# Kernel tuning notes

Measured on AMD Instinct MI355X. Metric: run time of the kernel, lower is better.

Reference implementation:

```python
import jax, jax.numpy as jnp
import numpy as np

H = 1024        # rnn_hidden
E = 128         # label_emb_dim
L = 17          # num_labels
START = L       # start-of-sequence label id


def setup_inputs() -> dict:
    key = jax.random.key(0)
    ks = jax.random.split(key, 8)
    B, T = 256, 512
    seg_encodings = jax.random.normal(ks[0], (B, T, H), jnp.float32)
    labels = jax.random.randint(ks[1], (B, T), 0, L, dtype=jnp.int32)
    def init(k, shape, fan_in):
        return (jax.random.normal(k, shape, jnp.float32) / np.sqrt(fan_in)).astype(jnp.float32)
    emb_table = init(ks[2], (L + 1, E), E)          # label_emb.weight
    W_ih = init(ks[3], (3 * H, H + E), H + E)        # gru.weight_ih_l0 (r,z,n)
    W_hh = init(ks[4], (3 * H, H), H)                # gru.weight_hh_l0
    b_ih = jnp.zeros((3 * H,), jnp.float32)
    b_hh = jnp.zeros((3 * H,), jnp.float32)
    W_out = init(ks[5], (L, H), H)                   # out.weight
    b_out = jnp.zeros((L,), jnp.float32)
    return {"seg_encodings": seg_encodings, "labels": labels,
            "emb_table": emb_table, "W_ih": W_ih, "W_hh": W_hh,
            "b_ih": b_ih, "b_hh": b_hh, "W_out": W_out, "b_out": b_out}


def reference(seg_encodings, labels, emb_table, W_ih, W_hh, b_ih, b_hh, W_out, b_out):
    B, T, _ = seg_encodings.shape
    # teacher forcing: prev label at step t is labels[:, t-1], START at t=0
    prev = jnp.concatenate([jnp.full((B, 1), START, labels.dtype), labels[:, :-1]], axis=1)
    prev_emb = emb_table[prev]                                  # [B,T,E]
    x = jnp.concatenate([seg_encodings, prev_emb], axis=-1)     # [B,T,H+E]
    # hoist the input projection out of the recurrence: one big GEMM
    x_proj = jnp.einsum('bti,gi->btg', x, W_ih) + b_ih          # [B,T,3H]

    def step(h, xp):                                            # h:[B,H], xp:[B,3H]
        gh = h @ W_hh.T + b_hh                                  # [B,3H]
        xr, xz, xn = jnp.split(xp, 3, axis=-1)
        hr, hz, hn = jnp.split(gh, 3, axis=-1)
        r = jax.nn.sigmoid(xr + hr)
        z = jax.nn.sigmoid(xz + hz)
        n = jnp.tanh(xn + r * hn)
        h_new = (1.0 - z) * n + z * h
        return h_new, h_new

    h0 = jnp.zeros((B, H), seg_encodings.dtype)
    _, hs = jax.lax.scan(step, h0, jnp.swapaxes(x_proj, 0, 1))  # hs: [T,B,H]
    hs = jnp.swapaxes(hs, 0, 1)                                 # [B,T,H]
    logits = jnp.einsum('bth,lh->btl', hs, W_out) + b_out       # [B,T,L]
    return logits
```

## Files before the change

### kernel.cpp

```cpp
#include <hip/hip_runtime.h>
#include <hip/hip_fp16.h>

typedef unsigned short u16;
typedef unsigned int u32;
typedef unsigned long long u64;

#define NT 512
#define NB 256
#define NH 1024
#define NE 128
#define NHE 1152
#define NL 17
#define MT 8
#define JTILES 32
#define XKC 36
#define HKC 32
#define KCT 68
#define NBLK 256
#define THREADS 512

typedef __attribute__((ext_vector_type(8))) _Float16 half8;
typedef __attribute__((ext_vector_type(4))) float f32x4;

#define WS_CNT     0ull
#define WS_HBUF    4096ull
#define WS_WPACK   1052672ull
#define WS_WOPACK  14422016ull
#define WS_XPACK   14487552ull
#define WS_TOTAL   316477440ull

#define HB_U64_PER (HKC * 2 * 64 * 2)
#define XSLOT_U16  (XKC * 2 * 64 * 8)

__device__ __forceinline__ u16 f2h(float f) {
  __half h = __float2half(f);
  return __builtin_bit_cast(u16, h);
}
__device__ __forceinline__ float h2f(u16 u) {
  return __half2float(__builtin_bit_cast(__half, u));
}
__device__ __forceinline__ uint4 pack8h(const u16* o) {
  uint4 v;
  v.x = (u32)o[0] | ((u32)o[1] << 16);
  v.y = (u32)o[2] | ((u32)o[3] << 16);
  v.z = (u32)o[4] | ((u32)o[5] << 16);
  v.w = (u32)o[6] | ((u32)o[7] << 16);
  return v;
}

__device__ __forceinline__ void gll16u(const void* g, void* l) {
  __builtin_amdgcn_global_load_lds((const __attribute__((address_space(1))) u32*)g,
                                   (__attribute__((address_space(3))) u32*)l, 16, 0, 17);
}
__device__ __forceinline__ void gll16c(const void* g, void* l) {
  __builtin_amdgcn_global_load_lds((const __attribute__((address_space(1))) u32*)g,
                                   (__attribute__((address_space(3))) u32*)l, 16, 0, 0);
}

__global__ void zero_ws(uint4* p) {
  int idx = blockIdx.x * 256 + threadIdx.x;
  if (idx < 33024) {
    uint4 z; z.x = 0; z.y = 0; z.z = 0; z.w = 0;
    p[idx] = z;
  }
}

__global__ void pack_w(const float* __restrict__ Wih, const float* __restrict__ Whh,
                       const float* __restrict__ Wout, u16* __restrict__ wpack,
                       u16* __restrict__ wopack) {
  int idx = blockIdx.x * 256 + threadIdx.x;
  const int WUNITS = JTILES * KCT * 3 * 2 * 64;
  if (idx < WUNITS) {
    int l = idx & 63;
    int r = idx >> 6;
    int ni = r & 1; r >>= 1;
    int g = r % 3;  r /= 3;
    int kc = r % KCT; r /= KCT;
    int jt = r;
    int row = g * NH + jt * 32 + ni * 16 + (l & 15);
    int kk = (l >> 4) * 8;
    const float* src = (kc < XKC) ? (Wih + (size_t)row * NHE + kc * 32 + kk)
                                  : (Whh + (size_t)row * NH + (kc - XKC) * 32 + kk);
    u16 o[8];
#pragma unroll
    for (int e = 0; e < 8; ++e) o[e] = f2h(src[e]);
    ((uint4*)wpack)[idx] = pack8h(o);
  } else if (idx < WUNITS + HKC * 2 * 64) {
    int j = idx - WUNITS;
    int l = j & 63; j >>= 6;
    int ni = j & 1; int kc = j >> 1;
    int col = (l & 15) + 16 * ni;
    int kk = kc * 32 + (l >> 4) * 8;
    u16 o[8];
#pragma unroll
    for (int e = 0; e < 8; ++e)
      o[e] = (col < NL) ? f2h(Wout[(size_t)col * NH + kk + e]) : (u16)0;
    ((uint4*)wopack)[idx - WUNITS] = pack8h(o);
  }
}

__global__ void pack_x(const float* __restrict__ seg, const int* __restrict__ labels,
                       const float* __restrict__ emb, u16* __restrict__ xpack) {
  __shared__ float ls[32][65];
  __shared__ int lbl[32];
  const int bid = blockIdx.x;
  const int t = bid & (NT - 1);
  const int m = bid >> 9;
  const int tid = threadIdx.x;
  u16* outb = xpack + (size_t)(m * NT + t) * XSLOT_U16;
  const int r = tid >> 3, qq = tid & 7;
  const int l = tid & 63;

  for (int kc2 = 0; kc2 < 16; ++kc2) {
    const float* s = seg + ((size_t)(m * 32 + r) * NT + t) * NH + kc2 * 64 + qq * 8;
    float4 a = ((const float4*)s)[0];
    float4 b2 = ((const float4*)s)[1];
    ls[r][qq * 8 + 0] = a.x;  ls[r][qq * 8 + 1] = a.y;
    ls[r][qq * 8 + 2] = a.z;  ls[r][qq * 8 + 3] = a.w;
    ls[r][qq * 8 + 4] = b2.x; ls[r][qq * 8 + 5] = b2.y;
    ls[r][qq * 8 + 6] = b2.z; ls[r][qq * 8 + 7] = b2.w;
    __syncthreads();
    const int sub2 = tid >> 6;
    const int kc = kc2 * 2 + (sub2 >> 1);
    const int sub = sub2 & 1;
    const int row = sub * 16 + (l & 15);
    const int c0 = (sub2 >> 1) * 32 + (l >> 4) * 8;
    u16 o[8];
#pragma unroll
    for (int e = 0; e < 8; ++e) o[e] = f2h(ls[row][c0 + e]);
    ((uint4*)outb)[(kc * 2 + sub) * 64 + l] = pack8h(o);
    __syncthreads();
  }
  if (tid < 32)
    lbl[tid] = (t == 0) ? NL : labels[(size_t)(m * 32 + tid) * NT + (t - 1)];
  __syncthreads();
#pragma unroll
  for (int k = 0; k < 2; ++k) {
    int u = tid + k * 256;
    int kc = 32 + (u >> 7);
    int sub = (u >> 6) & 1;
    int ll = u & 63;
    int row = sub * 16 + (ll & 15);
    int c = (kc - 32) * 32 + (ll >> 4) * 8;
    const float* s = emb + (size_t)lbl[row] * NE + c;
    float4 a = ((const float4*)s)[0];
    float4 b2 = ((const float4*)s)[1];
    u16 o[8];
    o[0] = f2h(a.x); o[1] = f2h(a.y); o[2] = f2h(a.z); o[3] = f2h(a.w);
    o[4] = f2h(b2.x); o[5] = f2h(b2.y); o[6] = f2h(b2.z); o[7] = f2h(b2.w);
    ((uint4*)outb)[(kc * 2 + sub) * 64 + ll] = pack8h(o);
  }
}

#define MFMA16(a, b, c) __builtin_amdgcn_mfma_f32_16x16x32_f16((a), (b), (c), 0, 0, 0)

#define WAIT_FLAGS(tgt) do { \
  while (true) { \
    u32 v_ = __hip_atomic_load(fl + (l & 31), __ATOMIC_RELAXED, __HIP_MEMORY_SCOPE_AGENT); \
    if (__all((int)v_ >= (tgt))) break; \
  } \
} while (0)

#define ISSUE_X(tt) do { \
  const char* xgb_ = (const char*)xpack + (size_t)(m * NT + (tt)) * (XSLOT_U16 * 2); \
  _Pragma("unroll") \
  for (int k_ = 0; k_ < 9; ++k_) \
    gll16c(xgb_ + ((size_t)(k_ * 512 + tid)) * 16, (void*)(xlds + (k_ * 512 + w * 64))); \
} while (0)

__global__ __launch_bounds__(THREADS, 1)
void gru_persist(u16* xpack, const u16* __restrict__ wpack,
                 const float* __restrict__ bih, const float* __restrict__ bhh,
                 u64* __restrict__ hbuf, u32* __restrict__ counters) {
  __shared__ uint4 hlds[HKC * 2 * 64];
  __shared__ uint4 xlds[XKC * 2 * 64];
  __shared__ u32 glds16[8 * 2 * 2 * 2 * 64];
  __shared__ u16 hbf[32 * 40];

  const int bid = blockIdx.x;
  const int xcd = bid & 7;
  const int q = bid >> 3;
  const int m = q & 7;
  const int jslot = q >> 3;
  const int jt = jslot * 8 + xcd;
  const int tid = threadIdx.x;
  const int w = tid >> 6, l = tid & 63;
  const int l15 = l & 15, l4 = l >> 4;
  const int usub = (w >> 1) & 1, uni = w & 1;

  const uint4* wp = (const uint4*)wpack;
  u32* fl = counters + m * 64;
  const size_t wbase_u = (size_t)jt * (KCT * 6 * 64);

  const int ocol = jt * 32 + uni * 16 + l15;
  const float br = bih[ocol] + bhh[ocol];
  const float bz = bih[NH + ocol] + bhh[NH + ocol];
  const float bxn = bih[2 * NH + ocol];
  const float bhn = bhh[2 * NH + ocol];
  float hold[4] = {0.f, 0.f, 0.f, 0.f};
  const f32x4 z4 = {0.f, 0.f, 0.f, 0.f};

  int tg, tkc0, tkcn; bool tIsX;
  if (w == 6)      { tg = 2; tIsX = true;  tkc0 = 0;  tkcn = 36; }
  else if (w == 7) { tg = 2; tIsX = false; tkc0 = 0;  tkcn = 32; }
  else {
    tg = (w < 3) ? 0 : 1;
    const int r_ = (w < 3) ? w : (w - 3);
    tIsX = (r_ < 2);
    tkc0 = (r_ == 1) ? 18 : 0;
    tkcn = tIsX ? ((r_ == 0) ? 18 : 36) : 32;
  }
  const int tkadd = tIsX ? 0 : XKC;
  const uint4* asrc = tIsX ? xlds : hlds;

  const int a_sub = (tid >> 7) & 1, a_half = (tid >> 6) & 1, a_l = tid & 63;
  const size_t a_off = ((size_t)(jt * 2 + a_sub) * 64 + a_l) * 2 + a_half;

  ISSUE_X(0);

  for (int t = 0; t < NT; ++t) {
    const int par = t & 1;

    WAIT_FLAGS(t);

    {
      const char* gb = (const char*)hbuf + ((size_t)(par * MT + m) * HB_U64_PER) * 8;
#pragma unroll
      for (int k = 0; k < 8; ++k)
        gll16u(gb + ((size_t)(k * 512 + tid)) * 16, (void*)(hlds + (k * 512 + w * 64)));
      asm volatile("s_waitcnt vmcnt(0)" ::: "memory");
      __syncthreads();
    }

    if (t > 0 && tid < 256) {
      const u64 v = ((const u64*)hlds)[a_off];
      u64* dst = (u64*)(xpack + (size_t)(m * NT + (t - 1)) * XSLOT_U16);
      dst[a_off] = v;
    }

    f32x4 acc[2][2];
    acc[0][0] = z4; acc[0][1] = z4; acc[1][0] = z4; acc[1][1] = z4;
#pragma unroll 4
    for (int kc = tkc0; kc < tkcn; ++kc) {
      const int kcw = kc + tkadd;
      uint4 A0 = asrc[(kc * 2 + 0) * 64 + l];
      uint4 A1 = asrc[(kc * 2 + 1) * 64 + l];
      uint4 B0 = wp[wbase_u + (size_t)((kcw * 3 + tg) * 2 + 0) * 64 + l];
      uint4 B1 = wp[wbase_u + (size_t)((kcw * 3 + tg) * 2 + 1) * 64 + l];
      half8 a0 = __builtin_bit_cast(half8, A0);
      half8 a1 = __builtin_bit_cast(half8, A1);
      half8 b0 = __builtin_bit_cast(half8, B0);
      half8 b1 = __builtin_bit_cast(half8, B1);
      acc[0][0] = MFMA16(a0, b0, acc[0][0]);
      acc[0][1] = MFMA16(a0, b1, acc[0][1]);
      acc[1][0] = MFMA16(a1, b0, acc[1][0]);
      acc[1][1] = MFMA16(a1, b1, acc[1][1]);
    }

#pragma unroll
    for (int s = 0; s < 2; ++s)
#pragma unroll
      for (int n = 0; n < 2; ++n)
#pragma unroll
        for (int rgp = 0; rgp < 2; ++rgp) {
          u32 v = (u32)f2h(acc[s][n][rgp * 2]) |
                  ((u32)f2h(acc[s][n][rgp * 2 + 1]) << 16);
          glds16[((((w * 2 + s) * 2 + n) * 2 + rgp)) * 64 + l] = v;
        }
    __syncthreads();

    if (w < 4) {
      float gv[8][4];
#pragma unroll
      for (int task = 0; task < 8; ++task)
#pragma unroll
        for (int rgp = 0; rgp < 2; ++rgp) {
          u32 v = glds16[((((task * 2 + usub) * 2 + uni) * 2 + rgp)) * 64 + l];
          gv[task][rgp * 2]     = h2f((u16)v);
          gv[task][rgp * 2 + 1] = h2f((u16)(v >> 16));
        }
#pragma unroll
      for (int rg = 0; rg < 4; ++rg) {
        float R   = gv[0][rg] + gv[1][rg] + gv[2][rg] + br;
        float Z   = gv[3][rg] + gv[4][rg] + gv[5][rg] + bz;
        float XNv = gv[6][rg] + bxn;
        float HNv = gv[7][rg] + bhn;
        float r_ = 1.f / (1.f + __expf(-R));
        float z_ = 1.f / (1.f + __expf(-Z));
        float pre = XNv + r_ * HNv;
        float e2 = __expf(2.f * pre);
        float n_ = 1.f - 2.f / (e2 + 1.f);
        float hn_ = (1.f - z_) * n_ + z_ * hold[rg];
        hold[rg] = hn_;
        hbf[(usub * 16 + l4 * 4 + rg) * 40 + uni * 16 + l15] = f2h(hn_);
      }
    }
    __syncthreads();

    if (w < 2) {
      const int row = w * 16 + l15;
      const uint4 hv = *(const uint4*)&hbf[(size_t)row * 40 + l4 * 8];
      u64 lo = ((u64)hv.y << 32) | (u64)hv.x;
      u64 hi = ((u64)hv.w << 32) | (u64)hv.z;
      u64* dst = hbuf + (size_t)((par ^ 1) * MT + m) * HB_U64_PER
                      + ((size_t)(jt * 2 + w) * 64 + l) * 2;
      __hip_atomic_store(dst, lo, __ATOMIC_RELAXED, __HIP_MEMORY_SCOPE_AGENT);
      __hip_atomic_store(dst + 1, hi, __ATOMIC_RELAXED, __HIP_MEMORY_SCOPE_AGENT);
    }
    asm volatile("s_waitcnt vmcnt(0)" ::: "memory");
    __syncthreads();
    if (tid == 0)
      __hip_atomic_store(fl + jt, (u32)(t + 1), __ATOMIC_RELAXED, __HIP_MEMORY_SCOPE_AGENT);

    if (t + 1 < NT) ISSUE_X(t + 1);
  }
}

__global__ __launch_bounds__(256, 1)
void logits_pass(const u16* __restrict__ harch, const u64* __restrict__ hbuf,
                 const u16* __restrict__ wopack, const float* __restrict__ bout,
                 float* __restrict__ out) {
  __shared__ uint4 hlds[HKC * 2 * 64];
  __shared__ f32x4 redv[4 * 3 * 64];
  const int bid = blockIdx.x;
  const int m = bid >> 9;
  const int s = bid & 511;
  const int tid = threadIdx.x;
  const int w = tid >> 6, l = tid & 63;
  const int l15 = l & 15, l4 = l >> 4;
  const int usub = w >> 1, uni = w & 1;
  const uint4* wo = (const uint4*)wopack;
  const f32x4 z4 = {0.f, 0.f, 0.f, 0.f};

  const char* gb = (s < 511)
      ? (const char*)(harch + (size_t)(m * NT + s) * XSLOT_U16)
      : (const char*)(hbuf + (size_t)(0 * MT + m) * HB_U64_PER);
#pragma unroll
  for (int k = 0; k < 16; ++k)
    gll16c(gb + ((size_t)(k * 256 + tid)) * 16, (void*)(hlds + (k * 256 + w * 64)));
  asm volatile("s_waitcnt vmcnt(0)" ::: "memory");
  __syncthreads();

  f32x4 aL[2][2];
  aL[0][0] = z4; aL[0][1] = z4; aL[1][0] = z4; aL[1][1] = z4;
#pragma unroll
  for (int c_ = 0; c_ < 8; ++c_) {
    const int kc_ = w * 8 + c_;
    uint4 A0 = hlds[(kc_ * 2 + 0) * 64 + l];
    uint4 A1 = hlds[(kc_ * 2 + 1) * 64 + l];
    uint4 O0 = wo[(size_t)(kc_ * 2 + 0) * 64 + l];
    uint4 O1 = wo[(size_t)(kc_ * 2 + 1) * 64 + l];
    half8 a0 = __builtin_bit_cast(half8, A0);
    half8 a1 = __builtin_bit_cast(half8, A1);
    half8 o0 = __builtin_bit_cast(half8, O0);
    half8 o1 = __builtin_bit_cast(half8, O1);
    aL[0][0] = MFMA16(a0, o0, aL[0][0]);
    aL[0][1] = MFMA16(a0, o1, aL[0][1]);
    aL[1][0] = MFMA16(a1, o0, aL[1][0]);
    aL[1][1] = MFMA16(a1, o1, aL[1][1]);
  }
  f32x4 sL;
#pragma unroll
  for (int o = 0; o < 4; ++o) {
    if (o == w) sL = aL[usub][uni];
    else {
      const int slot = (w > o) ? (w - 1) : w;
      redv[(o * 3 + slot) * 64 + l] = aL[o >> 1][o & 1];
    }
  }
  __syncthreads();
#pragma unroll
  for (int slot = 0; slot < 3; ++slot)
    sL += redv[(w * 3 + slot) * 64 + l];
  const int col = uni * 16 + l15;
  if (col < NL) {
#pragma unroll
    for (int rg = 0; rg < 4; ++rg) {
      const int row = usub * 16 + l4 * 4 + rg;
      const size_t b_ = (size_t)m * 32 + row;
      out[(b_ * NT + s) * NL + col] = sL[rg] + bout[col];
    }
  }
}

extern "C" void kernel_launch(void* const* d_in, const int* in_sizes, int n_in,
                              void* d_out, int out_size, void* d_ws, size_t ws_size,
                              hipStream_t stream) {
  (void)in_sizes; (void)n_in; (void)out_size;
  const float* seg   = (const float*)d_in[0];
  const int*   labels= (const int*)d_in[1];
  const float* emb   = (const float*)d_in[2];
  const float* Wih   = (const float*)d_in[3];
  const float* Whh   = (const float*)d_in[4];
  const float* bih   = (const float*)d_in[5];
  const float* bhh   = (const float*)d_in[6];
  const float* Wout  = (const float*)d_in[7];
  const float* bout  = (const float*)d_in[8];
  float* out = (float*)d_out;
  char* ws = (char*)d_ws;
  if (ws_size < WS_TOTAL) return;

  zero_ws<<<129, 256, 0, stream>>>((uint4*)(ws + WS_CNT));
  pack_w<<<3280, 256, 0, stream>>>(Wih, Whh, Wout,
                                   (u16*)(ws + WS_WPACK), (u16*)(ws + WS_WOPACK));
  pack_x<<<4096, 256, 0, stream>>>(seg, labels, emb, (u16*)(ws + WS_XPACK));
  gru_persist<<<NBLK, THREADS, 0, stream>>>(
      (u16*)(ws + WS_XPACK), (const u16*)(ws + WS_WPACK), bih, bhh,
      (u64*)(ws + WS_HBUF), (u32*)(ws + WS_CNT));
  logits_pass<<<MT * NT, 256, 0, stream>>>(
      (const u16*)(ws + WS_XPACK), (const u64*)(ws + WS_HBUF),
      (const u16*)(ws + WS_WOPACK), bout, out);
}
```

Before: 4.522 ms.

## Replace block barriers with LDS ready counters and warp-specialized H loading

Only the three waves that consume the hidden state now poll the cross-block flags and DMA h into LDS. The other waves wait on a workgroup-scope LDS counter that signals the x tile has landed, instead of taking part in block-wide __syncthreads around the h load and flag publish. The x prefetch for the next step is issued right after the gate reduction barrier, and a single wave does the h writeback and flag store. This is meant to let the x-side MFMA work start before the cross-block dependency resolves and to cut barrier stalls. It relies on spin loops over LDS atomics, which adds contention and memory-ordering risk.

```diff
diff --git a/kernel.cpp b/kernel.cpp
--- a/kernel.cpp
+++ b/kernel.cpp
@@ -161,13 +161,6 @@
   } \
 } while (0)
 
-#define ISSUE_X(tt) do { \
-  const char* xgb_ = (const char*)xpack + (size_t)(m * NT + (tt)) * (XSLOT_U16 * 2); \
-  _Pragma("unroll") \
-  for (int k_ = 0; k_ < 9; ++k_) \
-    gll16c(xgb_ + ((size_t)(k_ * 512 + tid)) * 16, (void*)(xlds + (k_ * 512 + w * 64))); \
-} while (0)
-
 __global__ __launch_bounds__(THREADS, 1)
 void gru_persist(u16* xpack, const u16* __restrict__ wpack,
                  const float* __restrict__ bih, const float* __restrict__ bhh,
@@ -176,6 +169,7 @@
   __shared__ uint4 xlds[XKC * 2 * 64];
   __shared__ u32 glds16[8 * 2 * 2 * 2 * 64];
   __shared__ u16 hbf[32 * 40];
+  __shared__ u32 rdy[16];
 
   const int bid = blockIdx.x;
   const int xcd = bid & 7;
@@ -200,49 +194,67 @@
   float hold[4] = {0.f, 0.f, 0.f, 0.f};
   const f32x4 z4 = {0.f, 0.f, 0.f, 0.f};
 
-  int tg, tkc0, tkcn; bool tIsX;
-  if (w == 6)      { tg = 2; tIsX = true;  tkc0 = 0;  tkcn = 36; }
-  else if (w == 7) { tg = 2; tIsX = false; tkc0 = 0;  tkcn = 32; }
-  else {
-    tg = (w < 3) ? 0 : 1;
-    const int r_ = (w < 3) ? w : (w - 3);
-    tIsX = (r_ < 2);
-    tkc0 = (r_ == 1) ? 18 : 0;
-    tkcn = tIsX ? ((r_ == 0) ? 18 : 36) : 32;
-  }
-  const int tkadd = tIsX ? 0 : XKC;
-  const uint4* asrc = tIsX ? xlds : hlds;
-
-  const int a_sub = (tid >> 7) & 1, a_half = (tid >> 6) & 1, a_l = tid & 63;
-  const size_t a_off = ((size_t)(jt * 2 + a_sub) * 64 + a_l) * 2 + a_half;
-
-  ISSUE_X(0);
+  const bool isH = (w == 2) || (w == 5) || (w == 7);
+  const int tg = (w < 3) ? 0 : (w < 6) ? 1 : 2;
+  int kc0 = 0, kc1;
+  if (isH) kc1 = HKC;
+  else if (w == 6) kc1 = XKC;
+  else { kc0 = (w == 1 || w == 4) ? 18 : 0; kc1 = kc0 + 18; }
+  const int kcadd = isH ? XKC : 0;
+  const uint4* asrc = isH ? hlds : xlds;
+  int dma0 = 0, dman = 0;
+  if (w == 2) { dma0 = 0;  dman = 21; }
+  else if (w == 5) { dma0 = 21; dman = 42; }
+  else if (w == 7) { dma0 = 42; dman = 64; }
+
+  if (tid == 0) { rdy[0] = 0; rdy[1] = 0; }
+  __syncthreads();
+  {
+    const char* xgb = (const char*)xpack + (size_t)(m * NT) * (XSLOT_U16 * 2);
+#pragma unroll
+    for (int j = 0; j < 9; ++j) {
+      const int c = w * 9 + j;
+      gll16c(xgb + (size_t)c * 1024 + (size_t)l * 16, (void*)(xlds + c * 64));
+    }
+    asm volatile("s_waitcnt vmcnt(0)" ::: "memory");
+    if (l == 0)
+      __hip_atomic_fetch_add(&rdy[0], 1u, __ATOMIC_RELEASE, __HIP_MEMORY_SCOPE_WORKGROUP);
+  }
 
   for (int t = 0; t < NT; ++t) {
     const int par = t & 1;
 
-    WAIT_FLAGS(t);
-
-    {
+    if (isH) {
+      WAIT_FLAGS(t);
       const char* gb = (const char*)hbuf + ((size_t)(par * MT + m) * HB_U64_PER) * 8;
-#pragma unroll
-      for (int k = 0; k < 8; ++k)
-        gll16u(gb + ((size_t)(k * 512 + tid)) * 16, (void*)(hlds + (k * 512 + w * 64)));
+      for (int u = dma0; u < dman; ++u)
+        gll16u(gb + (size_t)u * 1024 + (size_t)l * 16, (void*)(hlds + u * 64));
       asm volatile("s_waitcnt vmcnt(0)" ::: "memory");
-      __syncthreads();
-    }
-
-    if (t > 0 && tid < 256) {
-      const u64 v = ((const u64*)hlds)[a_off];
-      u64* dst = (u64*)(xpack + (size_t)(m * NT + (t - 1)) * XSLOT_U16);
-      dst[a_off] = v;
+      if (l == 0)
+        __hip_atomic_fetch_add(&rdy[1], 1u, __ATOMIC_RELEASE, __HIP_MEMORY_SCOPE_WORKGROUP);
+      while (__hip_atomic_load(&rdy[1], __ATOMIC_ACQUIRE, __HIP_MEMORY_SCOPE_WORKGROUP)
+             < 3u * (u32)(t + 1)) {}
+      __builtin_amdgcn_sched_barrier(0);
+    } else {
+      while (__hip_atomic_load(&rdy[0], __ATOMIC_ACQUIRE, __HIP_MEMORY_SCOPE_WORKGROUP)
+             < 8u * (u32)(t + 1)) {}
+      __builtin_amdgcn_sched_barrier(0);
+    }
+
+    if (w == 5 && t > 0) {
+      uint4* adst = (uint4*)(xpack + (size_t)(m * NT + (t - 1)) * XSLOT_U16);
+#pragma unroll
+      for (int s = 0; s < 2; ++s) {
+        const int u = jt * 2 + s;
+        adst[u * 64 + l] = hlds[u * 64 + l];
+      }
     }
 
     f32x4 acc[2][2];
     acc[0][0] = z4; acc[0][1] = z4; acc[1][0] = z4; acc[1][1] = z4;
 #pragma unroll 4
-    for (int kc = tkc0; kc < tkcn; ++kc) {
-      const int kcw = kc + tkadd;
+    for (int kc = kc0; kc < kc1; ++kc) {
+      const int kcw = kc + kcadd;
       uint4 A0 = asrc[(kc * 2 + 0) * 64 + l];
       uint4 A1 = asrc[(kc * 2 + 1) * 64 + l];
       uint4 B0 = wp[wbase_u + (size_t)((kcw * 3 + tg) * 2 + 0) * 64 + l];
@@ -268,6 +280,15 @@
           glds16[((((w * 2 + s) * 2 + n) * 2 + rgp)) * 64 + l] = v;
         }
     __syncthreads();
+
+    if (t + 1 < NT) {
+      const char* xgb = (const char*)xpack + (size_t)(m * NT + (t + 1)) * (XSLOT_U16 * 2);
+#pragma unroll
+      for (int j = 0; j < 9; ++j) {
+        const int c = w * 9 + j;
+        gll16c(xgb + (size_t)c * 1024 + (size_t)l * 16, (void*)(xlds + c * 64));
+      }
+    }
 
     if (w < 4) {
       float gv[8][4];
@@ -297,22 +318,26 @@
     }
     __syncthreads();
 
-    if (w < 2) {
-      const int row = w * 16 + l15;
-      const uint4 hv = *(const uint4*)&hbf[(size_t)row * 40 + l4 * 8];
-      u64 lo = ((u64)hv.y << 32) | (u64)hv.x;
-      u64 hi = ((u64)hv.w << 32) | (u64)hv.z;
-      u64* dst = hbuf + (size_t)((par ^ 1) * MT + m) * HB_U64_PER
-                      + ((size_t)(jt * 2 + w) * 64 + l) * 2;
-      __hip_atomic_store(dst, lo, __ATOMIC_RELAXED, __HIP_MEMORY_SCOPE_AGENT);
-      __hip_atomic_store(dst + 1, hi, __ATOMIC_RELAXED, __HIP_MEMORY_SCOPE_AGENT);
-    }
+    if (w == 7) {
+      u64* dst = hbuf + (size_t)((par ^ 1) * MT + m) * HB_U64_PER;
+#pragma unroll
+      for (int s = 0; s < 2; ++s) {
+        const int row = s * 16 + l15;
+        const uint4 hv = *(const uint4*)&hbf[(size_t)row * 40 + l4 * 8];
+        u64 lo = ((u64)hv.y << 32) | (u64)hv.x;
+        u64 hi = ((u64)hv.w << 32) | (u64)hv.z;
+        const size_t o_ = ((size_t)(jt * 2 + s) * 64 + l) * 2;
+        __hip_atomic_store(dst + o_,     lo, __ATOMIC_RELAXED, __HIP_MEMORY_SCOPE_AGENT);
+        __hip_atomic_store(dst + o_ + 1, hi, __ATOMIC_RELAXED, __HIP_MEMORY_SCOPE_AGENT);
+      }
+      asm volatile("s_waitcnt vmcnt(0)" ::: "memory");
+      if (l == 0)
+        __hip_atomic_store(fl + jt, (u32)(t + 1), __ATOMIC_RELAXED, __HIP_MEMORY_SCOPE_AGENT);
+    }
+
     asm volatile("s_waitcnt vmcnt(0)" ::: "memory");
-    __syncthreads();
-    if (tid == 0)
-      __hip_atomic_store(fl + jt, (u32)(t + 1), __ATOMIC_RELAXED, __HIP_MEMORY_SCOPE_AGENT);
-
-    if (t + 1 < NT) ISSUE_X(t + 1);
+    if (l == 0)
+      __hip_atomic_fetch_add(&rdy[0], 1u, __ATOMIC_RELEASE, __HIP_MEMORY_SCOPE_WORKGROUP);
   }
 }
 
```

New measurement: 4.860 ms. 1.07x slower.
